# Kernel tuning notes

Hardware: AMD Instinct MI355X
Metric: run time of the kernel (lower is better)

Reference implementation:

```python
import jax, jax.numpy as jnp
import numpy as np
from jax import lax

C, HID, NCLS, CDIM = 16, 128, 32, 64

def _dwconv(x, k):
    # x: [B,C,H,W], k: [C,1,3,3] depthwise (groups=C), SAME padding
    return lax.conv_general_dilated(
        x, k, window_strides=(1, 1), padding='SAME',
        dimension_numbers=('NCHW', 'OIHW', 'NCHW'), feature_group_count=x.shape[1])

def setup_inputs() -> dict:
    key = jax.random.key(0)
    ks = jax.random.split(key, 10)
    B, H, W = 4, 256, 256
    Fin = 3 * C
    inp = {
        'x': jax.random.normal(ks[0], (B, C, H, W), jnp.float32),
        'cond': jax.random.randint(ks[1], (B,), 0, NCLS, jnp.int32),
        'embed': jax.random.normal(ks[2], (NCLS, CDIM), jnp.float32) * 0.1,
        # Linear weights stored as [in, out] (transposed torch layout)
        'film_w': jax.random.normal(ks[3], (CDIM, 2 * HID), jnp.float32) * (1.0 / np.sqrt(CDIM)),
        'film_b': jnp.zeros((2 * HID,), jnp.float32),
        'fc1_w': jax.random.normal(ks[4], (Fin, HID), jnp.float32) * (1.0 / np.sqrt(Fin)),
        'fc1_b': jnp.zeros((HID,), jnp.float32),
        'fc2_w': jax.random.normal(ks[5], (HID, HID), jnp.float32) * (1.0 / np.sqrt(HID)),
        'fc2_b': jnp.zeros((HID,), jnp.float32),
        # fc3 is zero-init in the module; use small random values so output != input
        'fc3_w': jax.random.normal(ks[6], (HID, C), jnp.float32) * 0.01,
        'fc3_b': jnp.zeros((C,), jnp.float32),
        'n_steps': 4,
    }
    return inp

def reference(x, cond, embed, film_w, film_b, fc1_w, fc1_b, fc2_w, fc2_b, fc3_w, fc3_b, n_steps):
    sx = jnp.array([[-1., 0., 1.], [-2., 0., 2.], [-1., 0., 1.]], jnp.float32)
    kx = jnp.tile(sx[None, None], (C, 1, 1, 1))   # [C,1,3,3]
    ky = jnp.tile(sx.T[None, None], (C, 1, 1, 1))

    # FiLM params are step-invariant: compute once
    film = embed[cond] @ film_w + film_b          # [B, 2*HID]
    gamma, beta = jnp.split(film, 2, axis=1)      # [B, HID] each
    gamma = gamma[:, None, None, :]               # [B,1,1,HID]
    beta = beta[:, None, None, :]

    def step(xs, _):
        gx = _dwconv(xs, kx)
        gy = _dwconv(xs, ky)
        feats = jnp.concatenate([xs, gx, gy], axis=1).transpose(0, 2, 3, 1)  # [B,H,W,3C]
        h = jax.nn.relu(feats @ fc1_w + fc1_b)
        h = gamma * h + beta
        h = jax.nn.relu(h @ fc2_w + fc2_b)
        dx = (h @ fc3_w + fc3_b).transpose(0, 3, 1, 2)                        # [B,C,H,W]
        dx = jnp.clip(dx, -10.0, 10.0)
        return xs + dx * 0.1, None

    out, _ = lax.scan(step, x, None, length=n_steps)
    return out
```

## Files before the change

kernel.cpp:

```cpp
#include <hip/hip_runtime.h>

typedef __bf16 bf16x8 __attribute__((ext_vector_type(8)));
typedef float f32x4 __attribute__((ext_vector_type(4)));
typedef float f32x16 __attribute__((ext_vector_type(16)));
typedef unsigned int u32x4 __attribute__((ext_vector_type(4)));

#define FILM_WS 0
#define W1_WS   4096
#define W2B_WS  20480
#define W3_WS   151552
#define B2_WS   159744
#define XBUF_WS 163840

#define W1_OFF  0
#define W2_OFF  16384
#define W3_OFF  49152
#define XL_OFF  57344
#define LDS_TOTAL 92160

static __device__ __forceinline__ unsigned short f2bf(float f) {
  unsigned int u = __builtin_bit_cast(unsigned int, f);
  u += 0x7fffu + ((u >> 16) & 1u);
  return (unsigned short)(u >> 16);
}

static __device__ __forceinline__ unsigned cvtpk(float lo, float hi) {
  unsigned r;
  asm("v_cvt_pk_bf16_f32 %0, %1, %2" : "=v"(r) : "v"(lo), "v"(hi));
  return r;
}

static __device__ __forceinline__ void plswap(unsigned &a, unsigned &b) {
  auto r = __builtin_amdgcn_permlane32_swap((int)a, (int)b, false, false);
  a = (unsigned)r[0];
  b = (unsigned)r[1];
}

static __device__ __forceinline__ f32x16 MF(bf16x8 a, bf16x8 b, f32x16 c) {
  return __builtin_amdgcn_mfma_f32_32x32x16_bf16(a, b, c, 0, 0, 0);
}

template <int OFF>
static __device__ __forceinline__ u32x4 cvt2(f32x16 a) {
  unsigned A0 = cvtpk(fmaxf(a[OFF + 0], 0.f), fmaxf(a[OFF + 1], 0.f));
  unsigned A1 = cvtpk(fmaxf(a[OFF + 2], 0.f), fmaxf(a[OFF + 3], 0.f));
  unsigned B0 = cvtpk(fmaxf(a[OFF + 4], 0.f), fmaxf(a[OFF + 5], 0.f));
  unsigned B1 = cvtpk(fmaxf(a[OFF + 6], 0.f), fmaxf(a[OFF + 7], 0.f));
  plswap(A0, B0); plswap(A1, B1);
  return (u32x4){A0, A1, B0, B1};
}

#define ZERO16 (f32x16){0.f,0.f,0.f,0.f,0.f,0.f,0.f,0.f,0.f,0.f,0.f,0.f,0.f,0.f,0.f,0.f}
#define LDW(off) __builtin_bit_cast(bf16x8, *(const u32x4*)(sm + (off)))
#define U2B(v)   __builtin_bit_cast(bf16x8, v)

__global__ __launch_bounds__(256) void prep_film(
    const int* __restrict__ cond, const float* __restrict__ embed,
    const float* __restrict__ film_w, const float* __restrict__ film_b,
    char* __restrict__ ws) {
  int id = blockIdx.x * 256 + threadIdx.x;
  int b = id >> 8, j = id & 255;
  const float* e = embed + cond[b] * 64;
  float s = film_b[j];
  #pragma unroll 8
  for (int k = 0; k < 64; ++k) s += e[k] * film_w[k * 256 + j];
  ((float*)(ws + FILM_WS))[b * 256 + j] = s;
}

__global__ __launch_bounds__(256) void prep_w(
    const float* __restrict__ fc1w, const float* __restrict__ fc1b,
    const float* __restrict__ fc2w, const float* __restrict__ fc2b,
    const float* __restrict__ fc3w, char* __restrict__ ws) {
  int id = blockIdx.x * 256 + threadIdx.x;
  const float* film = (const float*)(ws + FILM_WS);
  if (id < 8192) {
    int n = id >> 6, k = id & 63;
    float v = (k < 48) ? fc1w[k * 128 + n] : (k == 48 ? fc1b[n] : 0.f);
    *(unsigned short*)(ws + W1_WS + ((n * 128 + 2 * k) ^ ((n & 7) << 4))) = f2bf(v);
  } else if (id < 8192 + 65536) {
    int t = id - 8192; int bb = t >> 14; t &= 16383;
    int n = t >> 7, k = t & 127;
    float v = film[bb * 256 + k] * fc2w[k * 128 + n];
    *(unsigned short*)(ws + W2B_WS + bb * 32768 + ((n * 256 + 2 * k) ^ ((n & 15) << 4))) = f2bf(v);
  } else if (id < 8192 + 65536 + 4096) {
    int t = id - 73728; int n = t >> 7, k = t & 127;
    float v = (n < 16) ? fc3w[k * 16 + n] : 0.f;
    *(unsigned short*)(ws + W3_WS + ((n * 256 + 2 * k) ^ ((n & 15) << 4))) = f2bf(v);
  } else if (id < 8192 + 65536 + 4096 + 512) {
    int t = id - 77824; int bb = t >> 7, n = t & 127;
    float s = fc2b[n];
    #pragma unroll 8
    for (int k = 0; k < 128; ++k)
      s += film[bb * 256 + 128 + k] * fc2w[k * 128 + n];
    ((float*)(ws + B2_WS))[bb * 128 + n] = s;
  }
}

#define G1NT(nt, ZA, ZB) do {                                               \
    const int n_ = (nt) * 32 + l31;                                         \
    const int rb_ = n_ * 128, sw_ = (n_ & 7) << 4;                          \
    bf16x8 wA_ = LDW(W1_OFF + ((rb_ +  0 + 16 * h5) ^ sw_));                \
    bf16x8 wB_ = LDW(W1_OFF + ((rb_ + 32 + 16 * h5) ^ sw_));                \
    bf16x8 wC_ = LDW(W1_OFF + ((rb_ + 64 + 16 * h5) ^ sw_));                \
    bf16x8 wD_ = LDW(W1_OFF + ((rb_ + 96 + 16 * h5) ^ sw_));                \
    f32x16 a_ = ZERO16;                                                     \
    a_ = MF(wA_, fx,  a_);                                                  \
    a_ = MF(wB_, fgx, a_);                                                  \
    a_ = MF(wC_, fgy, a_);                                                  \
    a_ = MF(wD_, fone, a_);                                                 \
    ZA = cvt2<0>(a_); ZB = cvt2<8>(a_);                                     \
  } while (0)

#define K2(kk) do {                                                         \
    bf16x8 wf_ = LDW(W2_OFF + ((rb2_ + 32 * (kk) + 16 * h5) ^ sw2_));       \
    a_ = MF(wf_, U2B(z##kk), a_);                                           \
  } while (0)

#define G23NT(nt) do {                                                      \
    const int n_ = (nt) * 32 + l31;                                         \
    const int rb2_ = n_ * 256, sw2_ = (n_ & 15) << 4;                       \
    f32x16 a_ = ZERO16;                                                     \
    K2(0); K2(1); K2(2); K2(3); K2(4); K2(5); K2(6); K2(7);                 \
    bf16x8 wb_ = U2B(((u32x4){wb2##nt, 0u, 0u, 0u}));                       \
    a_ = MF(wb_, fone, a_);                                                 \
    u32x4 hA_ = cvt2<0>(a_), hB_ = cvt2<8>(a_);                             \
    bf16x8 w3a_ = LDW(W3_OFF + ((rb3 + 32 * (2 * (nt))     + 16 * h5) ^ sw3)); \
    bf16x8 w3b_ = LDW(W3_OFF + ((rb3 + 32 * (2 * (nt) + 1) + 16 * h5) ^ sw3)); \
    cacc = MF(w3a_, U2B(hA_), cacc);                                        \
    cacc = MF(w3b_, U2B(hB_), cacc);                                        \
  } while (0)

__global__ __launch_bounds__(512)
__attribute__((amdgpu_waves_per_eu(2, 2)))
void step_kernel(
    const float* __restrict__ xin, float* __restrict__ xout,
    const char* __restrict__ ws, const float* __restrict__ fc3b) {
  __shared__ __attribute__((aligned(16))) char sm[LDS_TOTAL];
  float* smf = (float*)(sm + XL_OFF);
  const int tid = threadIdx.x;
  const int bid = blockIdx.x;
  const int b = bid >> 6, idx = bid & 63;

  for (int i = tid; i < 3584; i += 512) {
    const char* src; int dst;
    if (i < 1024)      { src = ws + W1_WS + i * 16;                       dst = W1_OFF + i * 16; }
    else if (i < 3072) { src = ws + W2B_WS + b * 32768 + (i - 1024) * 16; dst = W2_OFF + (i - 1024) * 16; }
    else               { src = ws + W3_WS + (i - 3072) * 16;              dst = W3_OFF + (i - 3072) * 16; }
    *(u32x4*)(sm + dst) = *(const u32x4*)src;
  }

  const int lane = tid & 63, wv = tid >> 6;
  const int l31 = lane & 31, h5 = lane >> 5;
  const int p = wv * 32 + l31;
  const int pr = p >> 7, pc = p & 127;
  const int cbase = h5 * 8;
  const unsigned bONE = (h5 == 0) ? 0x3F80u : 0u;
  const bf16x8 fone = U2B(((u32x4){bONE, 0u, 0u, 0u}));
  const int rb3 = l31 * 256, sw3 = (l31 & 15) << 4;

  const float* b2p = (const float*)(ws + B2_WS) + b * 128 + l31;
  const unsigned wb20 = (h5 == 0) ? cvtpk(b2p[0],  0.f) : 0u;
  const unsigned wb21 = (h5 == 0) ? cvtpk(b2p[32], 0.f) : 0u;
  const unsigned wb22 = (h5 == 0) ? cvtpk(b2p[64], 0.f) : 0u;
  const unsigned wb23 = (h5 == 0) ? cvtpk(b2p[96], 0.f) : 0u;
  const float b3v = (l31 < 16) ? fc3b[l31] : 0.f;
  const unsigned wb3 = (h5 == 0) ? cvtpk(b3v, 0.f) : 0u;

  const int iseg = tid >> 5, iq = tid & 31;
  const int eseg = tid >> 1, ee = tid & 1;

  f32x4 pre0, pre1, pre2, pre3;
  float peg;
  auto PREFETCH = [&](int jn) {
    const int h0n = idx * 4 + (jn >> 1) * 2;
    const int w0n = (jn & 1) << 7;
    #define HLOAD(T, K) do {                                                \
        int seg_ = iseg + 16 * (K);                                         \
        int c_ = seg_ >> 2, dh_ = seg_ & 3;                                 \
        int g_ = h0n - 1 + dh_;                                             \
        T = (f32x4){0.f, 0.f, 0.f, 0.f};                                    \
        if ((unsigned)g_ < 256u)                                            \
          T = *(const f32x4*)(xin + (((b * 16 + c_) * 256 + g_) << 8) + w0n + 4 * iq); \
      } while (0)
    HLOAD(pre0, 0); HLOAD(pre1, 1); HLOAD(pre2, 2); HLOAD(pre3, 3);
    #undef HLOAD
    peg = 0.f;
    if (tid < 128) {
      int c_ = eseg >> 2, dh_ = eseg & 3;
      int g_ = h0n - 1 + dh_;
      int w_ = w0n - 1 + ee * 129;
      if ((unsigned)g_ < 256u && (unsigned)w_ < 256u)
        peg = xin[(((b * 16 + c_) * 256 + g_) << 8) + w_];
    }
  };

  PREFETCH(0);

  #pragma unroll
  for (int j = 0; j < 4; ++j) {
    const int h0 = idx * 4 + (j >> 1) * 2;
    const int w0 = (j & 1) << 7;
    __syncthreads();
    *(f32x4*)(smf + (iseg +  0) * 136 + 4 + 4 * iq) = pre0;
    *(f32x4*)(smf + (iseg + 16) * 136 + 4 + 4 * iq) = pre1;
    *(f32x4*)(smf + (iseg + 32) * 136 + 4 + 4 * iq) = pre2;
    *(f32x4*)(smf + (iseg + 48) * 136 + 4 + 4 * iq) = pre3;
    if (tid < 128)
      smf[eseg * 136 + 3 + ee * 129] = peg;
    __syncthreads();

    if (j < 3) PREFETCH(j + 1);

    bf16x8 fx, fgx, fgy;
    #pragma unroll
    for (int jc = 0; jc < 8; ++jc) {
      const float* s0 = smf + ((cbase + jc) * 4 + pr) * 136 + 3 + pc;
      float a00 = s0[0],   a01 = s0[1],   a02 = s0[2];
      float a10 = s0[136], a11 = s0[137], a12 = s0[138];
      float a20 = s0[272], a21 = s0[273], a22 = s0[274];
      fx[jc]  = (__bf16)a11;
      fgx[jc] = (__bf16)((a02 - a00) + 2.f * (a12 - a10) + (a22 - a20));
      fgy[jc] = (__bf16)((a20 - a00) + 2.f * (a21 - a01) + (a22 - a02));
    }

    u32x4 z0, z1, z2, z3, z4, z5, z6, z7;
    G1NT(0, z0, z1);
    G1NT(1, z2, z3);
    G1NT(2, z4, z5);
    G1NT(3, z6, z7);

    f32x16 cacc = ZERO16;
    G23NT(0); G23NT(1); G23NT(2); G23NT(3);
    {
      bf16x8 wb_ = U2B(((u32x4){wb3, 0u, 0u, 0u}));
      cacc = MF(wb_, fone, cacc);
    }

    #pragma unroll
    for (int r = 0; r < 8; ++r) {
      const int c = 4 * h5 + (r & 3) + 8 * (r >> 2);
      float dx = fminf(fmaxf(cacc[r], -10.f), 10.f);
      float xo = smf[(c * 4 + pr + 1) * 136 + 4 + pc];
      xout[(((b * 16 + c) * 256 + h0 + pr) << 8) + w0 + pc] = xo + 0.1f * dx;
    }
  }
}

extern "C" void kernel_launch(void* const* d_in, const int* in_sizes, int n_in,
                              void* d_out, int out_size, void* d_ws, size_t ws_size,
                              hipStream_t stream) {
  const float* x      = (const float*)d_in[0];
  const int*   cond   = (const int*)d_in[1];
  const float* embed  = (const float*)d_in[2];
  const float* film_w = (const float*)d_in[3];
  const float* film_b = (const float*)d_in[4];
  const float* fc1w   = (const float*)d_in[5];
  const float* fc1b   = (const float*)d_in[6];
  const float* fc2w   = (const float*)d_in[7];
  const float* fc2b   = (const float*)d_in[8];
  const float* fc3w   = (const float*)d_in[9];
  const float* fc3b   = (const float*)d_in[10];

  char*  ws   = (char*)d_ws;
  float* xbuf = (float*)(ws + XBUF_WS);
  float* out  = (float*)d_out;

  prep_film<<<4, 256, 0, stream>>>(cond, embed, film_w, film_b, ws);
  prep_w<<<306, 256, 0, stream>>>(fc1w, fc1b, fc2w, fc2b, fc3w, ws);

  dim3 grid(256), blk(512);
  step_kernel<<<grid, blk, 0, stream>>>(x,    xbuf, ws, fc3b);
  step_kernel<<<grid, blk, 0, stream>>>(xbuf, out,  ws, fc3b);
  step_kernel<<<grid, blk, 0, stream>>>(out,  xbuf, ws, fc3b);
  step_kernel<<<grid, blk, 0, stream>>>(xbuf, out,  ws, fc3b);
}
```

Baseline: 113.5 us.

## Fuse four step launches into one cooperative kernel with grid sync

Replaces the four separate step kernel launches with a single cooperative kernel that loops over the steps, separated by grid-wide syncs. Weights stay resident in LDS across steps instead of being reloaded per launch, and the halo tile staging is double-buffered in LDS so one barrier per tile can be dropped. The costs are extra LDS use, grid.sync overhead between steps, and the requirement that all 256 blocks be co-resident for the cooperative launch.

```diff
diff --git a/kernel.cpp b/kernel.cpp
--- a/kernel.cpp
+++ b/kernel.cpp
@@ -1,4 +1,7 @@
 #include <hip/hip_runtime.h>
+#include <hip/hip_cooperative_groups.h>
+
+namespace cg = cooperative_groups;
 
 typedef __bf16 bf16x8 __attribute__((ext_vector_type(8)));
 typedef float f32x4 __attribute__((ext_vector_type(4)));
@@ -15,8 +18,9 @@
 #define W1_OFF  0
 #define W2_OFF  16384
 #define W3_OFF  49152
-#define XL_OFF  57344
-#define LDS_TOTAL 92160
+#define XL0_OFF 57344
+#define XL1_OFF 92160
+#define LDS_TOTAL 126976
 
 static __device__ __forceinline__ unsigned short f2bf(float f) {
   unsigned int u = __builtin_bit_cast(unsigned int, f);
@@ -132,11 +136,13 @@
 
 __global__ __launch_bounds__(512)
 __attribute__((amdgpu_waves_per_eu(2, 2)))
-void step_kernel(
-    const float* __restrict__ xin, float* __restrict__ xout,
-    const char* __restrict__ ws, const float* __restrict__ fc3b) {
+void step4_kernel(
+    const float* __restrict__ x0, float* __restrict__ xbuf,
+    float* __restrict__ xout, const char* __restrict__ ws,
+    const float* __restrict__ fc3b) {
   __shared__ __attribute__((aligned(16))) char sm[LDS_TOTAL];
-  float* smf = (float*)(sm + XL_OFF);
+  float* smf0 = (float*)(sm + XL0_OFF);
+  float* smf1 = (float*)(sm + XL1_OFF);
   const int tid = threadIdx.x;
   const int bid = blockIdx.x;
   const int b = bid >> 6, idx = bid & 63;
@@ -171,78 +177,92 @@
 
   f32x4 pre0, pre1, pre2, pre3;
   float peg;
-  auto PREFETCH = [&](int jn) {
-    const int h0n = idx * 4 + (jn >> 1) * 2;
-    const int w0n = (jn & 1) << 7;
-    #define HLOAD(T, K) do {                                                \
-        int seg_ = iseg + 16 * (K);                                         \
-        int c_ = seg_ >> 2, dh_ = seg_ & 3;                                 \
-        int g_ = h0n - 1 + dh_;                                             \
-        T = (f32x4){0.f, 0.f, 0.f, 0.f};                                    \
-        if ((unsigned)g_ < 256u)                                            \
-          T = *(const f32x4*)(xin + (((b * 16 + c_) * 256 + g_) << 8) + w0n + 4 * iq); \
-      } while (0)
-    HLOAD(pre0, 0); HLOAD(pre1, 1); HLOAD(pre2, 2); HLOAD(pre3, 3);
-    #undef HLOAD
-    peg = 0.f;
-    if (tid < 128) {
-      int c_ = eseg >> 2, dh_ = eseg & 3;
-      int g_ = h0n - 1 + dh_;
-      int w_ = w0n - 1 + ee * 129;
-      if ((unsigned)g_ < 256u && (unsigned)w_ < 256u)
-        peg = xin[(((b * 16 + c_) * 256 + g_) << 8) + w_];
+  cg::grid_group grid = cg::this_grid();
+
+  #pragma unroll 1
+  for (int s = 0; s < 4; ++s) {
+    const float* xin = (s == 0) ? x0 : ((s == 2) ? xout : xbuf);
+    float*       xo  = (s & 1) ? xout : xbuf;
+
+    auto PRE = [&](int jn) {
+      const int h0n = idx * 4 + (jn >> 1) * 2;
+      const int w0n = (jn & 1) << 7;
+      #define HLOAD(T, K) do {                                              \
+          int seg_ = iseg + 16 * (K);                                       \
+          int c_ = seg_ >> 2, dh_ = seg_ & 3;                               \
+          int g_ = h0n - 1 + dh_;                                           \
+          T = (f32x4){0.f, 0.f, 0.f, 0.f};                                  \
+          if ((unsigned)g_ < 256u)                                          \
+            T = *(const f32x4*)(xin + (((b * 16 + c_) * 256 + g_) << 8) + w0n + 4 * iq); \
+        } while (0)
+      HLOAD(pre0, 0); HLOAD(pre1, 1); HLOAD(pre2, 2); HLOAD(pre3, 3);
+      #undef HLOAD
+      peg = 0.f;
+      if (tid < 128) {
+        int c_ = eseg >> 2, dh_ = eseg & 3;
+        int g_ = h0n - 1 + dh_;
+        int w_ = ((jn & 1) << 7) - 1 + ee * 129;
+        if ((unsigned)g_ < 256u && (unsigned)w_ < 256u)
+          peg = xin[(((b * 16 + c_) * 256 + g_) << 8) + w_];
+      }
+    };
+    auto WR = [&](float* dst) {
+      *(f32x4*)(dst + (iseg +  0) * 136 + 4 + 4 * iq) = pre0;
+      *(f32x4*)(dst + (iseg + 16) * 136 + 4 + 4 * iq) = pre1;
+      *(f32x4*)(dst + (iseg + 32) * 136 + 4 + 4 * iq) = pre2;
+      *(f32x4*)(dst + (iseg + 48) * 136 + 4 + 4 * iq) = pre3;
+      if (tid < 128)
+        dst[eseg * 136 + 3 + ee * 129] = peg;
+    };
+
+    PRE(0); WR(smf0);
+    __syncthreads();
+    #pragma unroll
+    for (int j = 0; j < 4; ++j) {
+      const int h0 = idx * 4 + (j >> 1) * 2;
+      const int w0 = (j & 1) << 7;
+      float* cur = (j & 1) ? smf1 : smf0;
+      float* nxt = (j & 1) ? smf0 : smf1;
+
+      if (j < 3) PRE(j + 1);
+
+      bf16x8 fx, fgx, fgy;
+      #pragma unroll
+      for (int jc = 0; jc < 8; ++jc) {
+        const float* s0 = cur + ((cbase + jc) * 4 + pr) * 136 + 3 + pc;
+        float a00 = s0[0],   a01 = s0[1],   a02 = s0[2];
+        float a10 = s0[136], a11 = s0[137], a12 = s0[138];
+        float a20 = s0[272], a21 = s0[273], a22 = s0[274];
+        fx[jc]  = (__bf16)a11;
+        fgx[jc] = (__bf16)((a02 - a00) + 2.f * (a12 - a10) + (a22 - a20));
+        fgy[jc] = (__bf16)((a20 - a00) + 2.f * (a21 - a01) + (a22 - a02));
+      }
+
+      u32x4 z0, z1, z2, z3, z4, z5, z6, z7;
+      G1NT(0, z0, z1);
+      G1NT(1, z2, z3);
+      G1NT(2, z4, z5);
+      G1NT(3, z6, z7);
+
+      if (j < 3) WR(nxt);
+
+      f32x16 cacc = ZERO16;
+      G23NT(0); G23NT(1); G23NT(2); G23NT(3);
+      {
+        bf16x8 wb_ = U2B(((u32x4){wb3, 0u, 0u, 0u}));
+        cacc = MF(wb_, fone, cacc);
+      }
+
+      #pragma unroll
+      for (int r = 0; r < 8; ++r) {
+        const int c = 4 * h5 + (r & 3) + 8 * (r >> 2);
+        float dx = fminf(fmaxf(cacc[r], -10.f), 10.f);
+        float xold = cur[(c * 4 + pr + 1) * 136 + 4 + pc];
+        xo[(((b * 16 + c) * 256 + h0 + pr) << 8) + w0 + pc] = xold + 0.1f * dx;
+      }
+      __syncthreads();
     }
-  };
-
-  PREFETCH(0);
-
-  #pragma unroll
-  for (int j = 0; j < 4; ++j) {
-    const int h0 = idx * 4 + (j >> 1) * 2;
-    const int w0 = (j & 1) << 7;
-    __syncthreads();
-    *(f32x4*)(smf + (iseg +  0) * 136 + 4 + 4 * iq) = pre0;
-    *(f32x4*)(smf + (iseg + 16) * 136 + 4 + 4 * iq) = pre1;
-    *(f32x4*)(smf + (iseg + 32) * 136 + 4 + 4 * iq) = pre2;
-    *(f32x4*)(smf + (iseg + 48) * 136 + 4 + 4 * iq) = pre3;
-    if (tid < 128)
-      smf[eseg * 136 + 3 + ee * 129] = peg;
-    __syncthreads();
-
-    if (j < 3) PREFETCH(j + 1);
-
-    bf16x8 fx, fgx, fgy;
-    #pragma unroll
-    for (int jc = 0; jc < 8; ++jc) {
-      const float* s0 = smf + ((cbase + jc) * 4 + pr) * 136 + 3 + pc;
-      float a00 = s0[0],   a01 = s0[1],   a02 = s0[2];
-      float a10 = s0[136], a11 = s0[137], a12 = s0[138];
-      float a20 = s0[272], a21 = s0[273], a22 = s0[274];
-      fx[jc]  = (__bf16)a11;
-      fgx[jc] = (__bf16)((a02 - a00) + 2.f * (a12 - a10) + (a22 - a20));
-      fgy[jc] = (__bf16)((a20 - a00) + 2.f * (a21 - a01) + (a22 - a02));
-    }
-
-    u32x4 z0, z1, z2, z3, z4, z5, z6, z7;
-    G1NT(0, z0, z1);
-    G1NT(1, z2, z3);
-    G1NT(2, z4, z5);
-    G1NT(3, z6, z7);
-
-    f32x16 cacc = ZERO16;
-    G23NT(0); G23NT(1); G23NT(2); G23NT(3);
-    {
-      bf16x8 wb_ = U2B(((u32x4){wb3, 0u, 0u, 0u}));
-      cacc = MF(wb_, fone, cacc);
-    }
-
-    #pragma unroll
-    for (int r = 0; r < 8; ++r) {
-      const int c = 4 * h5 + (r & 3) + 8 * (r >> 2);
-      float dx = fminf(fmaxf(cacc[r], -10.f), 10.f);
-      float xo = smf[(c * 4 + pr + 1) * 136 + 4 + pc];
-      xout[(((b * 16 + c) * 256 + h0 + pr) << 8) + w0 + pc] = xo + 0.1f * dx;
-    }
+    if (s < 3) grid.sync();
   }
 }
 
@@ -268,9 +288,8 @@
   prep_film<<<4, 256, 0, stream>>>(cond, embed, film_w, film_b, ws);
   prep_w<<<306, 256, 0, stream>>>(fc1w, fc1b, fc2w, fc2b, fc3w, ws);
 
-  dim3 grid(256), blk(512);
-  step_kernel<<<grid, blk, 0, stream>>>(x,    xbuf, ws, fc3b);
-  step_kernel<<<grid, blk, 0, stream>>>(xbuf, out,  ws, fc3b);
-  step_kernel<<<grid, blk, 0, stream>>>(out,  xbuf, ws, fc3b);
-  step_kernel<<<grid, blk, 0, stream>>>(xbuf, out,  ws, fc3b);
-}
+  const char* wsc = ws;
+  void* args[] = {(void*)&x, (void*)&xbuf, (void*)&out, (void*)&wsc, (void*)&fc3b};
+  hipLaunchCooperativeKernel((void*)step4_kernel, dim3(256), dim3(512),
+                             args, 0, stream);
+}
```

After: 222.9 us. +96.3%, slower.
